# Kernel optimization log

Hardware: AMD Instinct MI355X
Metric: run time of the kernel (lower is better)

Reference implementation:

```python
import math
import jax, jax.numpy as jnp
import numpy as np

DIM = 256
HEADS = 8
WS = (8, 8)   # window_size
SS = (4, 4)   # shift_size


def _rel_tables():
    """Static SwinV2 continuous relative-position coordinate table and index."""
    wh, ww = WS
    ch = np.arange(-(wh - 1), wh, dtype=np.float32)
    cw = np.arange(-(ww - 1), ww, dtype=np.float32)
    table = np.stack(np.meshgrid(ch, cw, indexing='ij'), axis=-1)  # (2wh-1, 2ww-1, 2)
    table[..., 0] /= (wh - 1)
    table[..., 1] /= (ww - 1)
    table *= 8.0
    table = np.sign(table) * np.log2(np.abs(table) + 1.0) / 3.0
    coords = np.stack(np.meshgrid(np.arange(wh), np.arange(ww), indexing='ij'))
    cf = coords.reshape(2, -1)                      # (2, N)
    rel = (cf[:, :, None] - cf[:, None, :]).transpose(1, 2, 0)  # (N, N, 2)
    rel[..., 0] += wh - 1
    rel[..., 1] += ww - 1
    rel[..., 0] *= 2 * ww - 1
    idx = rel.sum(-1).reshape(-1)                   # (N*N,)
    return jnp.asarray(table, jnp.float32), jnp.asarray(idx, jnp.int32)


def _attn_mask(pad_H, pad_W, sh, sw):
    """Static shifted-window attention mask, shape (num_windows, N, N)."""
    wh, ww = WS
    m = np.zeros((pad_H, pad_W), np.float32)
    cnt = 0
    for hs in ((0, -wh), (-wh, -sh), (-sh, None)):
        for ws_ in ((0, -ww), (-ww, -sw), (-sw, None)):
            m[hs[0]:hs[1], ws_[0]:ws_[1]] = cnt
            cnt += 1
    m = m.reshape(pad_H // wh, wh, pad_W // ww, ww).transpose(0, 2, 1, 3)
    m = m.reshape(-1, wh * ww)                      # (nW, N)
    diff = m[:, None, :] - m[:, :, None]            # (nW, N, N)
    return jnp.asarray(np.where(diff != 0, -100.0, 0.0).astype(np.float32))


def setup_inputs() -> dict:
    key = jax.random.key(0)
    ks = jax.random.split(key, 12)
    C, Hh = DIM, HEADS
    s = 0.02
    inp = {
        'x': jax.random.normal(ks[0], (16, 64, 64, C), jnp.float32),
        'Wq': jax.random.normal(ks[1], (C, C), jnp.float32) * s,
        'bq': jnp.zeros((C,), jnp.float32),
        'Wk': jax.random.normal(ks[2], (C, C), jnp.float32) * s,
        'bk': jnp.zeros((C,), jnp.float32),
        'Wv': jax.random.normal(ks[3], (C, C), jnp.float32) * s,
        'bv': jnp.zeros((C,), jnp.float32),
        'Wo': jax.random.normal(ks[4], (C, C), jnp.float32) * s,
        'bo': jnp.zeros((C,), jnp.float32),
        'logit_scale': jnp.full((Hh, 1, 1), math.log(10.0), jnp.float32),
        'cpb_w1': jax.random.normal(ks[5], (2, 512), jnp.float32) * s,
        'cpb_b1': jnp.zeros((512,), jnp.float32),
        'cpb_w2': jax.random.normal(ks[6], (512, Hh), jnp.float32) * s,
    }
    return inp


def reference(x, Wq, bq, Wk, bk, Wv, bv, Wo, bo, logit_scale, cpb_w1, cpb_b1, cpb_w2):
    B, H, W, C = x.shape
    wh, ww = WS
    hd = C // HEADS
    pad_b = (wh - H % wh) % wh
    pad_r = (ww - W % ww) % ww
    x = jnp.pad(x, ((0, 0), (0, pad_b), (0, pad_r), (0, 0)))
    pH, pW = H + pad_b, W + pad_r
    sh = 0 if wh >= pH else SS[0]
    sw = 0 if ww >= pW else SS[1]

    xs = jnp.roll(x, (-sh, -sw), axis=(1, 2))
    nW = (pH // wh) * (pW // ww)
    N = wh * ww
    # window partition -> (B*nW, N, C)
    xw = xs.reshape(B, pH // wh, wh, pW // ww, ww, C).transpose(0, 1, 3, 2, 4, 5)
    xw = xw.reshape(B * nW, N, C)

    def heads(t):
        return t.reshape(B * nW, N, HEADS, hd).transpose(0, 2, 1, 3)  # (BnW, H, N, hd)

    q = heads(xw @ Wq + bq)
    k = heads(xw @ Wk + bk)
    v = heads(xw @ Wv + bv)

    # cosine attention (F.normalize, eps=1e-12)
    qn = q / jnp.maximum(jnp.linalg.norm(q, axis=-1, keepdims=True), 1e-12)
    kn = k / jnp.maximum(jnp.linalg.norm(k, axis=-1, keepdims=True), 1e-12)
    attn = jnp.einsum('bhnd,bhmd->bhnm', qn, kn)

    scale = jnp.exp(jnp.minimum(logit_scale, math.log(100.0)))  # (HEADS,1,1)
    attn = attn * scale[None]

    table, idx = _rel_tables()
    bias = jax.nn.relu(table @ cpb_w1 + cpb_b1) @ cpb_w2        # (2wh-1, 2ww-1, HEADS)
    bias = bias.reshape(-1, HEADS)[idx].reshape(N, N, HEADS).transpose(2, 0, 1)
    attn = attn + (16.0 * jax.nn.sigmoid(bias))[None]

    if sh + sw > 0:
        mask = _attn_mask(pH, pW, sh, sw)                        # (nW, N, N)
        attn = attn.reshape(B, nW, HEADS, N, N) + mask[None, :, None]
        attn = attn.reshape(B * nW, HEADS, N, N)

    attn = jax.nn.softmax(attn, axis=-1)
    out = jnp.einsum('bhnm,bhmd->bhnd', attn, v)
    out = out.transpose(0, 2, 1, 3).reshape(B * nW, N, C)
    out = out @ Wo + bo

    out = out.reshape(B, pH // wh, pW // ww, wh, ww, C).transpose(0, 1, 3, 2, 4, 5)
    out = out.reshape(B, pH, pW, C)
    if sh + sw > 0:
        out = jnp.roll(out, (sh, sw), axis=(1, 2))
    return out[:, :H, :W, :]
```

## Files before the change

kernel.cpp:

```cpp
#include <hip/hip_runtime.h>
#include <hip/hip_bf16.h>

typedef float floatx4 __attribute__((ext_vector_type(4)));
typedef short shortx8 __attribute__((ext_vector_type(8)));
typedef short shortx4 __attribute__((ext_vector_type(4)));

#define CFENCE() asm volatile("" ::: "memory")

__device__ __forceinline__ float bf2f(short s) {
    union { unsigned u; float f; } cv;
    cv.u = ((unsigned)(unsigned short)s) << 16;
    return cv.f;
}
__device__ __forceinline__ short f2bf(float f) {
    union { float f; unsigned u; } cv; cv.f = f;
    unsigned r = (cv.u + 0x7fffu + ((cv.u >> 16) & 1u)) >> 16;
    return (short)r;
}

__global__ __launch_bounds__(256) void wtrans(const float* __restrict__ Wq,
                                              const float* __restrict__ Wk,
                                              const float* __restrict__ Wv,
                                              const float* __restrict__ Wo,
                                              short* __restrict__ wqkv_f,
                                              short* __restrict__ wo_f) {
    int gtid = blockIdx.x * 256 + threadIdx.x;
    int f = gtid >> 6, lane = gtid & 63;
    int quad = lane >> 4, l15 = lane & 15;
    if (f < 384) {
        int n16 = f >> 3, kt = f & 7;
        int n = n16 * 16 + l15, z = n >> 8, ncol = n & 255;
        const float* src = (z == 0) ? Wq : (z == 1) ? Wk : Wv;
        shortx8 s;
#pragma unroll
        for (int j = 0; j < 8; ++j)
            s[j] = f2bf(src[(size_t)(kt * 32 + quad * 8 + j) * 256 + ncol]);
        *(shortx8*)(wqkv_f + (size_t)f * 512 + lane * 8) = s;
    } else {
        int f2 = f - 384;
        int n16 = f2 >> 3, kt = f2 & 7;
        int n = n16 * 16 + l15;
        shortx8 s;
#pragma unroll
        for (int j = 0; j < 8; ++j)
            s[j] = f2bf(Wo[(size_t)(kt * 32 + quad * 8 + j) * 256 + n]);
        *(shortx8*)(wo_f + (size_t)f2 * 512 + lane * 8) = s;
    }
}

__device__ __forceinline__ float sgnlog(float x) {
    return copysignf(__log2f(fabsf(x) + 1.f) / 3.f, x);
}
__global__ __launch_bounds__(256) void bias_mlp(const float* __restrict__ ls,
                                                const float* __restrict__ w1,
                                                const float* __restrict__ b1,
                                                const float* __restrict__ w2,
                                                float* __restrict__ b225g,
                                                float* __restrict__ scaleOut) {
    int e = blockIdx.x;
    int tid = threadIdx.x, lane = tid & 63, wid = tid >> 6;
    if (e == 0 && tid < 8) scaleOut[tid] = expf(fminf(ls[tid], 4.6051701859880914f));
    int dh = e / 15 - 7, dw = e % 15 - 7;
    float t0 = sgnlog(8.f * (float)dh / 7.f);
    float t1 = sgnlog(8.f * (float)dw / 7.f);
    float acc[8];
#pragma unroll
    for (int j = 0; j < 8; ++j) acc[j] = 0.f;
#pragma unroll
    for (int s = 0; s < 2; ++s) {
        int hsm = tid + s * 256;
        float hid = fmaxf(0.f, t0 * w1[hsm] + t1 * w1[512 + hsm] + b1[hsm]);
#pragma unroll
        for (int j = 0; j < 8; ++j) acc[j] += hid * w2[hsm * 8 + j];
    }
#pragma unroll
    for (int off = 1; off < 64; off <<= 1)
#pragma unroll
        for (int j = 0; j < 8; ++j) acc[j] += __shfl_xor(acc[j], off, 64);
    __shared__ float red[4][8];
    if (lane == 0)
#pragma unroll
        for (int j = 0; j < 8; ++j) red[wid][j] = acc[j];
    __syncthreads();
    if (tid < 8)
        b225g[e * 8 + tid] = red[0][tid] + red[1][tid] + red[2][tid] + red[3][tid];
}

__global__ __launch_bounds__(256) void bias_expand(const float* __restrict__ b225g,
                                                   float* __restrict__ bias8) {
    int f = blockIdx.x * 256 + threadIdx.x;
    int h = f >> 12, ij = f & 4095, i = ij >> 6, j = ij & 63;
    int dh = (i >> 3) - (j >> 3), dw = (i & 7) - (j & 7);
    int e = (dh + 7) * 15 + (dw + 7);
    float v = b225g[e * 8 + h];
    bias8[f] = 16.f / (1.f + expf(-v));
}

__device__ __forceinline__ int row2pix(int row) {
    int w = row >> 6, t = row & 63;
    int b = w >> 6, wi = (w >> 3) & 7, wj = w & 7;
    int hh = (wi * 8 + (t >> 3) + 4) & 63;
    int ww = (wj * 8 + (t & 7) + 4) & 63;
    return (b * 64 + hh) * 64 + ww;
}

__global__ __launch_bounds__(256, 2) void qkv_gemm(const float* __restrict__ x,
                                                   const short* __restrict__ wf,
                                                   const float* __restrict__ bq,
                                                   const float* __restrict__ bk_,
                                                   const float* __restrict__ bv,
                                                   short* __restrict__ qkv2) {
    __shared__ __align__(16) short As[128 * 264];
    int tid = threadIdx.x, lane = tid & 63, wid = tid >> 6;
    int quad = lane >> 4, l15 = lane & 15;
    int bm = blockIdx.x;

    {
        int r = tid >> 1, half = tid & 1;
        const float* src = x + (size_t)row2pix(bm * 128 + r) * 256 + half * 128;
        short* dst = &As[r * 264 + half * 128];
#pragma unroll
        for (int g = 0; g < 4; ++g) {
            float4 v[8];
#pragma unroll
            for (int j = 0; j < 8; ++j) v[j] = *(const float4*)(src + g * 32 + j * 4);
#pragma unroll
            for (int j = 0; j < 4; ++j) {
                shortx8 s;
#pragma unroll
                for (int q2 = 0; q2 < 2; ++q2) {
                    float4 f = v[j * 2 + q2];
                    s[q2 * 4 + 0] = f2bf(f.x); s[q2 * 4 + 1] = f2bf(f.y);
                    s[q2 * 4 + 2] = f2bf(f.z); s[q2 * 4 + 3] = f2bf(f.w);
                }
                *(shortx8*)(dst + g * 32 + j * 8) = s;
            }
        }
    }

    int wm = (wid & 1) * 64, wnq = (wid >> 1);
    const short* bbase = wf + (size_t)wnq * 4 * 8 * 512 + lane * 8;

    shortx8 b0[4], b1[4];
#pragma unroll
    for (int nt = 0; nt < 4; ++nt)
        b0[nt] = *(const shortx8*)(bbase + ((size_t)nt * 8 + 0) * 512);
#pragma unroll
    for (int nt = 0; nt < 4; ++nt)
        b1[nt] = *(const shortx8*)(bbase + ((size_t)nt * 8 + 1) * 512);

    __syncthreads();

    for (int t = 0; t < 6; ++t) {
        floatx4 acc[4][4];
#pragma unroll
        for (int mt = 0; mt < 4; ++mt)
#pragma unroll
            for (int nt = 0; nt < 4; ++nt) acc[mt][nt] = (floatx4){0.f, 0.f, 0.f, 0.f};
#pragma unroll
        for (int kt = 0; kt < 8; ++kt) {
            int u = t * 8 + kt + 2;
            if (u > 47) u = 46;
            int tn = u >> 3, kn = u & 7;
            shortx8 bn[4];
#pragma unroll
            for (int nt = 0; nt < 4; ++nt)
                bn[nt] = *(const shortx8*)(bbase + ((size_t)(tn * 8 + wnq * 4 + nt) * 8 + kn) * 512 - (size_t)wnq * 4 * 8 * 512 + 0);
            shortx8 af[4];
#pragma unroll
            for (int mt = 0; mt < 4; ++mt)
                af[mt] = *(const shortx8*)&As[(wm + mt * 16 + l15) * 264 + kt * 32 + quad * 8];
#pragma unroll
            for (int mt = 0; mt < 4; ++mt)
#pragma unroll
                for (int nt = 0; nt < 4; ++nt)
                    acc[mt][nt] = __builtin_amdgcn_mfma_f32_16x16x32_bf16(af[mt], b0[nt], acc[mt][nt], 0, 0, 0);
#pragma unroll
            for (int nt = 0; nt < 4; ++nt) { b0[nt] = b1[nt]; b1[nt] = bn[nt]; }
        }
        float biasv[4];
        int colb[4];
#pragma unroll
        for (int nt = 0; nt < 4; ++nt) {
            int col = t * 128 + wnq * 64 + nt * 16 + l15;
            colb[nt] = col;
            biasv[nt] = (col < 256) ? bq[col] : (col < 512) ? bk_[col - 256] : bv[col - 512];
        }
#pragma unroll
        for (int mt = 0; mt < 4; ++mt)
#pragma unroll
            for (int reg = 0; reg < 4; ++reg) {
                int row = bm * 128 + wm + mt * 16 + quad * 4 + reg;
                int win = row >> 6, tok = row & 63;
                size_t rb = (size_t)win * 49152 + tok * 32;
#pragma unroll
                for (int nt = 0; nt < 4; ++nt) {
                    int col = colb[nt];
                    int qi = col >> 8, h = (col >> 5) & 7, d = col & 31;
                    qkv2[rb + (h * 3 + qi) * 2048 + d] = f2bf(acc[mt][nt][reg] + biasv[nt]);
                }
            }
    }
}

__device__ __forceinline__ int regid(int t, int wi, int wj) {
    int a = (wi < 7) ? 0 : (((t >> 3) < 4) ? 1 : 2);
    int b = (wj < 7) ? 0 : (((t & 7) < 4) ? 1 : 2);
    return a * 3 + b;
}

__global__ __launch_bounds__(256, 2) void attn_kernel(const short* __restrict__ qkv2,
                                                      const float* __restrict__ bias8,
                                                      const float* __restrict__ scale,
                                                      short* __restrict__ aout) {
    __shared__ __align__(16) short lds[4 * 8192];
    int tid = threadIdx.x, lane = tid & 63, wid = tid >> 6;
    int quad = lane >> 4, l15 = lane & 15;
    int win = blockIdx.x;
    int wi = (win >> 3) & 7, wj = win & 7;
    bool need_mask = (wi == 7) || (wj == 7);
    short* qn = &lds[wid * 8192];
    short* kn = qn + 3584;
    short* P = qn;
    short* vt = qn + 5632;

    for (int hi = 0; hi < 2; ++hi) {
        int h = wid + hi * 4;
        float sc = scale[h];
        const short* base = qkv2 + (size_t)(win * 8 + h) * 3 * 2048;
        shortx8 qraw[4], kraw[4], vraw[4];
#pragma unroll
        for (int c2 = 0; c2 < 4; ++c2) {
            qraw[c2] = *(const shortx8*)(base + lane * 32 + c2 * 8);
            kraw[c2] = *(const shortx8*)(base + 2048 + lane * 32 + c2 * 8);
            vraw[c2] = *(const shortx8*)(base + 4096 + lane * 32 + c2 * 8);
        }
        float qs = 0.f, ks2 = 0.f;
#pragma unroll
        for (int c2 = 0; c2 < 4; ++c2)
#pragma unroll
            for (int j = 0; j < 8; ++j) {
                float f = bf2f(qraw[c2][j]); qs += f * f;
                float g = bf2f(kraw[c2][j]); ks2 += g * g;
            }
        float qr = sc / fmaxf(sqrtf(qs), 1e-12f);
        float kr = 1.f / fmaxf(sqrtf(ks2), 1e-12f);
        CFENCE();
#pragma unroll
        for (int c2 = 0; c2 < 4; ++c2) {
            shortx8 oq, ok;
#pragma unroll
            for (int j = 0; j < 8; ++j) {
                oq[j] = f2bf(bf2f(qraw[c2][j]) * qr);
                ok[j] = f2bf(bf2f(kraw[c2][j]) * kr);
            }
            *(shortx8*)&qn[lane * 56 + c2 * 8] = oq;
            *(shortx8*)&kn[lane * 56 + c2 * 8] = ok;
        }
        CFENCE();
        shortx8 aq[4], bkf[4];
#pragma unroll
        for (int mt = 0; mt < 4; ++mt)
            aq[mt] = *(const shortx8*)&qn[(mt * 16 + l15) * 56 + quad * 8];
#pragma unroll
        for (int nt = 0; nt < 4; ++nt)
            bkf[nt] = *(const shortx8*)&kn[(nt * 16 + l15) * 56 + quad * 8];
        floatx4 S[4][4];
#pragma unroll
        for (int mt = 0; mt < 4; ++mt)
#pragma unroll
            for (int nt = 0; nt < 4; ++nt) {
                floatx4 z = {0.f, 0.f, 0.f, 0.f};
                S[mt][nt] = __builtin_amdgcn_mfma_f32_16x16x32_bf16(aq[mt], bkf[nt], z, 0, 0, 0);
            }
        const float* bh = bias8 + (h << 12);
        float bound = sc + 16.5f;
        int jid[4];
        if (need_mask) {
#pragma unroll
            for (int nt = 0; nt < 4; ++nt) jid[nt] = regid(nt * 16 + l15, wi, wj);
        }
        float rs[4][4];
#pragma unroll
        for (int mt = 0; mt < 4; ++mt)
#pragma unroll
            for (int reg = 0; reg < 4; ++reg) {
                int i = mt * 16 + quad * 4 + reg;
                int iid = need_mask ? regid(i, wi, wj) : 0;
                float rowsum = 0.f;
#pragma unroll
                for (int nt = 0; nt < 4; ++nt) {
                    int j = nt * 16 + l15;
                    float v = S[mt][nt][reg] + bh[i * 64 + j];
                    if (need_mask && iid != jid[nt]) v -= 100.f;
                    float p = __expf(v - bound);
                    S[mt][nt][reg] = p;
                    rowsum += p;
                }
                rowsum += __shfl_xor(rowsum, 1, 64);
                rowsum += __shfl_xor(rowsum, 2, 64);
                rowsum += __shfl_xor(rowsum, 4, 64);
                rowsum += __shfl_xor(rowsum, 8, 64);
                rs[mt][reg] = 1.f / rowsum;
            }
        CFENCE();
#pragma unroll
        for (int mt = 0; mt < 4; ++mt)
#pragma unroll
            for (int nt = 0; nt < 4; ++nt)
#pragma unroll
                for (int reg = 0; reg < 4; ++reg)
                    P[(mt * 16 + quad * 4 + reg) * 88 + nt * 16 + l15] = f2bf(S[mt][nt][reg]);
#pragma unroll
        for (int c2 = 0; c2 < 4; ++c2)
#pragma unroll
            for (int j = 0; j < 8; ++j)
                vt[(c2 * 8 + j) * 72 + lane] = vraw[c2][j];
        CFENCE();
        floatx4 O[4][2];
#pragma unroll
        for (int mt = 0; mt < 4; ++mt)
#pragma unroll
            for (int nt = 0; nt < 2; ++nt) O[mt][nt] = (floatx4){0.f, 0.f, 0.f, 0.f};
#pragma unroll
        for (int ks = 0; ks < 2; ++ks) {
            shortx8 pa[4], vb[2];
#pragma unroll
            for (int mt = 0; mt < 4; ++mt)
                pa[mt] = *(const shortx8*)&P[(mt * 16 + l15) * 88 + ks * 32 + quad * 8];
#pragma unroll
            for (int nt = 0; nt < 2; ++nt)
                vb[nt] = *(const shortx8*)&vt[(nt * 16 + l15) * 72 + ks * 32 + quad * 8];
#pragma unroll
            for (int mt = 0; mt < 4; ++mt)
#pragma unroll
                for (int nt = 0; nt < 2; ++nt)
                    O[mt][nt] = __builtin_amdgcn_mfma_f32_16x16x32_bf16(pa[mt], vb[nt], O[mt][nt], 0, 0, 0);
        }
#pragma unroll
        for (int mt = 0; mt < 4; ++mt)
#pragma unroll
            for (int nt = 0; nt < 2; ++nt)
#pragma unroll
                for (int reg = 0; reg < 4; ++reg) {
                    int i = mt * 16 + quad * 4 + reg;
                    int d = nt * 16 + l15;
                    aout[(size_t)(win * 64 + i) * 256 + (h << 5) + d] =
                        f2bf(O[mt][nt][reg] * rs[mt][reg]);
                }
    }
}

__global__ __launch_bounds__(256, 2) void oproj_gemm(const short* __restrict__ ao,
                                                     const short* __restrict__ wof,
                                                     const float* __restrict__ bo,
                                                     float* __restrict__ out) {
    __shared__ __align__(16) short As[128 * 264];
    int tid = threadIdx.x, lane = tid & 63, wid = tid >> 6;
    int quad = lane >> 4, l15 = lane & 15;
    int bm = blockIdx.x;

    {
        int r = tid >> 1, half = tid & 1;
        const short* src = ao + (size_t)(bm * 128 + r) * 256 + half * 128;
        short* dst = &As[r * 264 + half * 128];
#pragma unroll
        for (int g = 0; g < 2; ++g) {
            shortx8 v[8];
#pragma unroll
            for (int j = 0; j < 8; ++j) v[j] = *(const shortx8*)(src + g * 64 + j * 8);
#pragma unroll
            for (int j = 0; j < 8; ++j) *(shortx8*)(dst + g * 64 + j * 8) = v[j];
        }
    }

    int wm = (wid & 1) * 64, wnq = (wid >> 1);
    const short* bbase = wof + (size_t)wnq * 4 * 8 * 512 + lane * 8;

    shortx8 b0[4], b1[4];
#pragma unroll
    for (int nt = 0; nt < 4; ++nt)
        b0[nt] = *(const shortx8*)(bbase + ((size_t)nt * 8 + 0) * 512);
#pragma unroll
    for (int nt = 0; nt < 4; ++nt)
        b1[nt] = *(const shortx8*)(bbase + ((size_t)nt * 8 + 1) * 512);

    __syncthreads();

    for (int t = 0; t < 2; ++t) {
        floatx4 acc[4][4];
#pragma unroll
        for (int mt = 0; mt < 4; ++mt)
#pragma unroll
            for (int nt = 0; nt < 4; ++nt) acc[mt][nt] = (floatx4){0.f, 0.f, 0.f, 0.f};
#pragma unroll
        for (int kt = 0; kt < 8; ++kt) {
            int u = t * 8 + kt + 2;
            if (u > 15) u = 14;
            int tn = u >> 3, kn = u & 7;
            shortx8 bn[4];
#pragma unroll
            for (int nt = 0; nt < 4; ++nt)
                bn[nt] = *(const shortx8*)(bbase + ((size_t)(tn * 8 + nt) * 8 + kn) * 512);
            shortx8 af[4];
#pragma unroll
            for (int mt = 0; mt < 4; ++mt)
                af[mt] = *(const shortx8*)&As[(wm + mt * 16 + l15) * 264 + kt * 32 + quad * 8];
#pragma unroll
            for (int mt = 0; mt < 4; ++mt)
#pragma unroll
                for (int nt = 0; nt < 4; ++nt)
                    acc[mt][nt] = __builtin_amdgcn_mfma_f32_16x16x32_bf16(af[mt], b0[nt], acc[mt][nt], 0, 0, 0);
#pragma unroll
            for (int nt = 0; nt < 4; ++nt) { b0[nt] = b1[nt]; b1[nt] = bn[nt]; }
        }
        float biasv[4];
#pragma unroll
        for (int nt = 0; nt < 4; ++nt) biasv[nt] = bo[t * 128 + wnq * 64 + nt * 16 + l15];
#pragma unroll
        for (int mt = 0; mt < 4; ++mt)
#pragma unroll
            for (int nt = 0; nt < 4; ++nt)
#pragma unroll
                for (int reg = 0; reg < 4; ++reg) {
                    int row = bm * 128 + wm + mt * 16 + quad * 4 + reg;
                    int col = t * 128 + wnq * 64 + nt * 16 + l15;
                    out[(size_t)row2pix(row) * 256 + col] = acc[mt][nt][reg] + biasv[nt];
                }
    }
}

extern "C" void kernel_launch(void* const* d_in, const int* in_sizes, int n_in,
                              void* d_out, int out_size, void* d_ws, size_t ws_size,
                              hipStream_t stream) {
    const float* x  = (const float*)d_in[0];
    const float* Wq = (const float*)d_in[1];
    const float* bq = (const float*)d_in[2];
    const float* Wk = (const float*)d_in[3];
    const float* bk = (const float*)d_in[4];
    const float* Wv = (const float*)d_in[5];
    const float* bv = (const float*)d_in[6];
    const float* Wo = (const float*)d_in[7];
    const float* bo = (const float*)d_in[8];
    const float* ls = (const float*)d_in[9];
    const float* w1 = (const float*)d_in[10];
    const float* b1 = (const float*)d_in[11];
    const float* w2 = (const float*)d_in[12];

    char* ws = (char*)d_ws;
    short* wqkv_f = (short*)(ws + 0);
    short* wo_f   = (short*)(ws + 393216);
    float* bias8  = (float*)(ws + 524288);
    float* scale  = (float*)(ws + 655360);
    float* b225g  = (float*)(ws + 786432);
    short* qkv2   = (short*)(ws + 1048576);
    short* aout   = (short*)(ws + 101711872);
    float* out    = (float*)d_out;

    hipLaunchKernelGGL(wtrans, dim3(128), dim3(256), 0, stream, Wq, Wk, Wv, Wo, wqkv_f, wo_f);
    hipLaunchKernelGGL(bias_mlp, dim3(225), dim3(256), 0, stream, ls, w1, b1, w2, b225g, scale);
    hipLaunchKernelGGL(bias_expand, dim3(128), dim3(256), 0, stream, b225g, bias8);
    hipLaunchKernelGGL(qkv_gemm, dim3(512), dim3(256), 0, stream, x, wqkv_f, bq, bk, bv, qkv2);
    hipLaunchKernelGGL(attn_kernel, dim3(1024), dim3(256), 0, stream, qkv2, bias8, scale, aout);
    hipLaunchKernelGGL(oproj_gemm, dim3(512), dim3(256), 0, stream, aout, wo_f, bo, out);
}
```

Baseline: 249.6 us.

## Retile QKV and output-projection GEMMs to 64-row blocks with transposed MFMA for vector stores

Both projection GEMMs now use 64-row tiles (one window per block), which doubles the grid to 1024 blocks and raises the occupancy hint to 4 blocks per CU with half the LDS. The MFMA operands are swapped so each lane holds 4 consecutive output columns, which allows packed shortx4 stores into qkv2 and float4 stores into the output instead of scalar scattered writes. The register double-buffered weight prefetch is dropped in favour of direct per-k loads. In exchange, weights are reloaded by more blocks and global-load latency hiding now relies on occupancy rather than software pipelining.

```diff
diff --git a/kernel.cpp b/kernel.cpp
--- a/kernel.cpp
+++ b/kernel.cpp
@@ -104,23 +104,23 @@
     return (b * 64 + hh) * 64 + ww;
 }
 
-__global__ __launch_bounds__(256, 2) void qkv_gemm(const float* __restrict__ x,
+__global__ __launch_bounds__(256, 4) void qkv_gemm(const float* __restrict__ x,
                                                    const short* __restrict__ wf,
                                                    const float* __restrict__ bq,
                                                    const float* __restrict__ bk_,
                                                    const float* __restrict__ bv,
                                                    short* __restrict__ qkv2) {
-    __shared__ __align__(16) short As[128 * 264];
+    __shared__ __align__(16) short As[64 * 264];
     int tid = threadIdx.x, lane = tid & 63, wid = tid >> 6;
     int quad = lane >> 4, l15 = lane & 15;
-    int bm = blockIdx.x;
+    int win = blockIdx.x;
 
     {
-        int r = tid >> 1, half = tid & 1;
-        const float* src = x + (size_t)row2pix(bm * 128 + r) * 256 + half * 128;
-        short* dst = &As[r * 264 + half * 128];
-#pragma unroll
-        for (int g = 0; g < 4; ++g) {
+        int r = tid >> 2, q = tid & 3;
+        const float* src = x + (size_t)row2pix(win * 64 + r) * 256 + q * 64;
+        short* dst = &As[r * 264 + q * 64];
+#pragma unroll
+        for (int g = 0; g < 2; ++g) {
             float4 v[8];
 #pragma unroll
             for (int j = 0; j < 8; ++j) v[j] = *(const float4*)(src + g * 32 + j * 4);
@@ -138,68 +138,53 @@
         }
     }
 
-    int wm = (wid & 1) * 64, wnq = (wid >> 1);
-    const short* bbase = wf + (size_t)wnq * 4 * 8 * 512 + lane * 8;
-
-    shortx8 b0[4], b1[4];
-#pragma unroll
-    for (int nt = 0; nt < 4; ++nt)
-        b0[nt] = *(const shortx8*)(bbase + ((size_t)nt * 8 + 0) * 512);
-#pragma unroll
-    for (int nt = 0; nt < 4; ++nt)
-        b1[nt] = *(const shortx8*)(bbase + ((size_t)nt * 8 + 1) * 512);
+    const short* wbase = wf + lane * 8;
 
     __syncthreads();
 
-    for (int t = 0; t < 6; ++t) {
+    for (int t = 0; t < 3; ++t) {
+        int n16b = t * 16 + wid * 4;
         floatx4 acc[4][4];
 #pragma unroll
-        for (int mt = 0; mt < 4; ++mt)
-#pragma unroll
-            for (int nt = 0; nt < 4; ++nt) acc[mt][nt] = (floatx4){0.f, 0.f, 0.f, 0.f};
+        for (int nt = 0; nt < 4; ++nt)
+#pragma unroll
+            for (int mt = 0; mt < 4; ++mt) acc[nt][mt] = (floatx4){0.f, 0.f, 0.f, 0.f};
 #pragma unroll
         for (int kt = 0; kt < 8; ++kt) {
-            int u = t * 8 + kt + 2;
-            if (u > 47) u = 46;
-            int tn = u >> 3, kn = u & 7;
-            shortx8 bn[4];
+            shortx8 bw[4], af[4];
 #pragma unroll
             for (int nt = 0; nt < 4; ++nt)
-                bn[nt] = *(const shortx8*)(bbase + ((size_t)(tn * 8 + wnq * 4 + nt) * 8 + kn) * 512 - (size_t)wnq * 4 * 8 * 512 + 0);
-            shortx8 af[4];
+                bw[nt] = *(const shortx8*)(wbase + ((size_t)(n16b + nt) * 8 + kt) * 512);
 #pragma unroll
             for (int mt = 0; mt < 4; ++mt)
-                af[mt] = *(const shortx8*)&As[(wm + mt * 16 + l15) * 264 + kt * 32 + quad * 8];
-#pragma unroll
-            for (int mt = 0; mt < 4; ++mt)
-#pragma unroll
-                for (int nt = 0; nt < 4; ++nt)
-                    acc[mt][nt] = __builtin_amdgcn_mfma_f32_16x16x32_bf16(af[mt], b0[nt], acc[mt][nt], 0, 0, 0);
-#pragma unroll
-            for (int nt = 0; nt < 4; ++nt) { b0[nt] = b1[nt]; b1[nt] = bn[nt]; }
-        }
-        float biasv[4];
-        int colb[4];
+                af[mt] = *(const shortx8*)&As[(mt * 16 + l15) * 264 + kt * 32 + quad * 8];
+#pragma unroll
+            for (int nt = 0; nt < 4; ++nt)
+#pragma unroll
+                for (int mt = 0; mt < 4; ++mt)
+                    acc[nt][mt] = __builtin_amdgcn_mfma_f32_16x16x32_bf16(bw[nt], af[mt], acc[nt][mt], 0, 0, 0);
+        }
 #pragma unroll
         for (int nt = 0; nt < 4; ++nt) {
-            int col = t * 128 + wnq * 64 + nt * 16 + l15;
-            colb[nt] = col;
-            biasv[nt] = (col < 256) ? bq[col] : (col < 512) ? bk_[col - 256] : bv[col - 512];
-        }
-#pragma unroll
-        for (int mt = 0; mt < 4; ++mt)
+            int nb = (n16b + nt) * 16;
+            int qi = nb >> 8, h = (nb >> 5) & 7;
+            int db = (nb & 31) + quad * 4;
+            size_t slab = (size_t)win * 49152 + (size_t)(h * 3 + qi) * 2048;
+            float bs[4];
 #pragma unroll
             for (int reg = 0; reg < 4; ++reg) {
-                int row = bm * 128 + wm + mt * 16 + quad * 4 + reg;
-                int win = row >> 6, tok = row & 63;
-                size_t rb = (size_t)win * 49152 + tok * 32;
-#pragma unroll
-                for (int nt = 0; nt < 4; ++nt) {
-                    int col = colb[nt];
-                    int qi = col >> 8, h = (col >> 5) & 7, d = col & 31;
-                    qkv2[rb + (h * 3 + qi) * 2048 + d] = f2bf(acc[mt][nt][reg] + biasv[nt]);
-                }
-            }
+                int n = nb + quad * 4 + reg;
+                bs[reg] = (n < 256) ? bq[n] : (n < 512) ? bk_[n - 256] : bv[n - 512];
+            }
+#pragma unroll
+            for (int mt = 0; mt < 4; ++mt) {
+                int tok = mt * 16 + l15;
+                shortx4 s;
+#pragma unroll
+                for (int reg = 0; reg < 4; ++reg) s[reg] = f2bf(acc[nt][mt][reg] + bs[reg]);
+                *(shortx4*)(qkv2 + slab + tok * 32 + db) = s;
+            }
+        }
     }
 }
 
@@ -351,82 +336,67 @@
     }
 }
 
-__global__ __launch_bounds__(256, 2) void oproj_gemm(const short* __restrict__ ao,
+__global__ __launch_bounds__(256, 4) void oproj_gemm(const short* __restrict__ ao,
                                                      const short* __restrict__ wof,
                                                      const float* __restrict__ bo,
                                                      float* __restrict__ out) {
-    __shared__ __align__(16) short As[128 * 264];
+    __shared__ __align__(16) short As[64 * 264];
     int tid = threadIdx.x, lane = tid & 63, wid = tid >> 6;
     int quad = lane >> 4, l15 = lane & 15;
     int bm = blockIdx.x;
 
     {
-        int r = tid >> 1, half = tid & 1;
-        const short* src = ao + (size_t)(bm * 128 + r) * 256 + half * 128;
-        short* dst = &As[r * 264 + half * 128];
-#pragma unroll
-        for (int g = 0; g < 2; ++g) {
-            shortx8 v[8];
-#pragma unroll
-            for (int j = 0; j < 8; ++j) v[j] = *(const shortx8*)(src + g * 64 + j * 8);
-#pragma unroll
-            for (int j = 0; j < 8; ++j) *(shortx8*)(dst + g * 64 + j * 8) = v[j];
-        }
-    }
-
-    int wm = (wid & 1) * 64, wnq = (wid >> 1);
-    const short* bbase = wof + (size_t)wnq * 4 * 8 * 512 + lane * 8;
-
-    shortx8 b0[4], b1[4];
+        int r = tid >> 2, q = tid & 3;
+        const short* src = ao + (size_t)(bm * 64 + r) * 256 + q * 64;
+        short* dst = &As[r * 264 + q * 64];
+#pragma unroll
+        for (int j = 0; j < 8; ++j)
+            *(shortx8*)(dst + j * 8) = *(const shortx8*)(src + j * 8);
+    }
+
+    const short* wbase = wof + lane * 8;
+
+    __syncthreads();
+
+    floatx4 acc[4][4];
 #pragma unroll
     for (int nt = 0; nt < 4; ++nt)
-        b0[nt] = *(const shortx8*)(bbase + ((size_t)nt * 8 + 0) * 512);
-#pragma unroll
-    for (int nt = 0; nt < 4; ++nt)
-        b1[nt] = *(const shortx8*)(bbase + ((size_t)nt * 8 + 1) * 512);
-
-    __syncthreads();
-
-    for (int t = 0; t < 2; ++t) {
-        floatx4 acc[4][4];
-#pragma unroll
-        for (int mt = 0; mt < 4; ++mt)
-#pragma unroll
-            for (int nt = 0; nt < 4; ++nt) acc[mt][nt] = (floatx4){0.f, 0.f, 0.f, 0.f};
-#pragma unroll
-        for (int kt = 0; kt < 8; ++kt) {
-            int u = t * 8 + kt + 2;
-            if (u > 15) u = 14;
-            int tn = u >> 3, kn = u & 7;
-            shortx8 bn[4];
-#pragma unroll
-            for (int nt = 0; nt < 4; ++nt)
-                bn[nt] = *(const shortx8*)(bbase + ((size_t)(tn * 8 + nt) * 8 + kn) * 512);
-            shortx8 af[4];
+#pragma unroll
+        for (int mt = 0; mt < 4; ++mt) acc[nt][mt] = (floatx4){0.f, 0.f, 0.f, 0.f};
+#pragma unroll
+    for (int kt = 0; kt < 8; ++kt) {
+        shortx8 bw[4], af[4];
+#pragma unroll
+        for (int nt = 0; nt < 4; ++nt)
+            bw[nt] = *(const shortx8*)(wbase + ((size_t)(wid * 4 + nt) * 8 + kt) * 512);
+#pragma unroll
+        for (int mt = 0; mt < 4; ++mt)
+            af[mt] = *(const shortx8*)&As[(mt * 16 + l15) * 264 + kt * 32 + quad * 8];
+#pragma unroll
+        for (int nt = 0; nt < 4; ++nt)
 #pragma unroll
             for (int mt = 0; mt < 4; ++mt)
-                af[mt] = *(const shortx8*)&As[(wm + mt * 16 + l15) * 264 + kt * 32 + quad * 8];
-#pragma unroll
-            for (int mt = 0; mt < 4; ++mt)
-#pragma unroll
-                for (int nt = 0; nt < 4; ++nt)
-                    acc[mt][nt] = __builtin_amdgcn_mfma_f32_16x16x32_bf16(af[mt], b0[nt], acc[mt][nt], 0, 0, 0);
-#pragma unroll
-            for (int nt = 0; nt < 4; ++nt) { b0[nt] = b1[nt]; b1[nt] = bn[nt]; }
-        }
-        float biasv[4];
-#pragma unroll
-        for (int nt = 0; nt < 4; ++nt) biasv[nt] = bo[t * 128 + wnq * 64 + nt * 16 + l15];
-#pragma unroll
-        for (int mt = 0; mt < 4; ++mt)
-#pragma unroll
-            for (int nt = 0; nt < 4; ++nt)
-#pragma unroll
-                for (int reg = 0; reg < 4; ++reg) {
-                    int row = bm * 128 + wm + mt * 16 + quad * 4 + reg;
-                    int col = t * 128 + wnq * 64 + nt * 16 + l15;
-                    out[(size_t)row2pix(row) * 256 + col] = acc[mt][nt][reg] + biasv[nt];
-                }
+                acc[nt][mt] = __builtin_amdgcn_mfma_f32_16x16x32_bf16(bw[nt], af[mt], acc[nt][mt], 0, 0, 0);
+    }
+
+    int pix[4];
+#pragma unroll
+    for (int mt = 0; mt < 4; ++mt) pix[mt] = row2pix(bm * 64 + mt * 16 + l15);
+#pragma unroll
+    for (int nt = 0; nt < 4; ++nt) {
+        int nb = wid * 64 + nt * 16 + quad * 4;
+        float bs[4];
+#pragma unroll
+        for (int reg = 0; reg < 4; ++reg) bs[reg] = bo[nb + reg];
+#pragma unroll
+        for (int mt = 0; mt < 4; ++mt) {
+            float4 o;
+            o.x = acc[nt][mt][0] + bs[0];
+            o.y = acc[nt][mt][1] + bs[1];
+            o.z = acc[nt][mt][2] + bs[2];
+            o.w = acc[nt][mt][3] + bs[3];
+            *(float4*)(out + (size_t)pix[mt] * 256 + nb) = o;
+        }
     }
 }
 
@@ -460,7 +430,7 @@
     hipLaunchKernelGGL(wtrans, dim3(128), dim3(256), 0, stream, Wq, Wk, Wv, Wo, wqkv_f, wo_f);
     hipLaunchKernelGGL(bias_mlp, dim3(225), dim3(256), 0, stream, ls, w1, b1, w2, b225g, scale);
     hipLaunchKernelGGL(bias_expand, dim3(128), dim3(256), 0, stream, b225g, bias8);
-    hipLaunchKernelGGL(qkv_gemm, dim3(512), dim3(256), 0, stream, x, wqkv_f, bq, bk, bv, qkv2);
+    hipLaunchKernelGGL(qkv_gemm, dim3(1024), dim3(256), 0, stream, x, wqkv_f, bq, bk, bv, qkv2);
     hipLaunchKernelGGL(attn_kernel, dim3(1024), dim3(256), 0, stream, qkv2, bias8, scale, aout);
-    hipLaunchKernelGGL(oproj_gemm, dim3(512), dim3(256), 0, stream, aout, wo_f, bo, out);
-}
+    hipLaunchKernelGGL(oproj_gemm, dim3(1024), dim3(256), 0, stream, aout, wo_f, bo, out);
+}
```

After: 327.0 us. 1.31x slower.
